# Performance work log

Measured on AMD Instinct MI355X. Metric: run time of the kernel, lower is better.

## Reference

```python
import jax, jax.numpy as jnp
import numpy as np

TAU_PRE = 2.0
TAU_POST = 2.0


def setup_inputs() -> dict:
    key = jax.random.key(0)
    k1, k2, k3 = jax.random.split(key, 3)
    T, B, PRE, POST = 64, 16, 4096, 4096
    in_spikes = jax.random.uniform(k1, (T, B, PRE), dtype=jnp.float32)
    out_spikes = jax.random.uniform(k2, (T, B, POST), dtype=jnp.float32)
    weight = jax.random.normal(k3, (POST, PRE), dtype=jnp.float32)
    return {"in_spikes": in_spikes, "out_spikes": out_spikes, "weight": weight}


def reference(in_spikes, out_spikes, weight):
    # in_spikes: [T, B, pre]; out_spikes: [T, B, post]; weight: [post, pre]
    T, B, PRE = in_spikes.shape
    POST = out_spikes.shape[-1]

    def step(carry, xs):
        trace_pre, trace_post, delta_w = carry
        i_sp, o_sp = xs
        trace_pre = jnp.clip(trace_pre - trace_pre / TAU_PRE + i_sp, 0.0, 1.0)  # [B, pre]
        trace_post = trace_post - trace_post / TAU_POST + o_sp  # [B, post]
        # sum_b o[b,post]*trace_pre[b,pre] - (sum_b o[b,post]*trace_post[b,post]) * w[post,pre]
        dw = (jnp.einsum('bo,bp->op', o_sp, trace_pre)
              - (o_sp * trace_post).sum(0)[:, None] * weight)
        return (trace_pre, trace_post, delta_w + dw), None

    init = (jnp.zeros((B, PRE), in_spikes.dtype),
            jnp.zeros((B, POST), out_spikes.dtype),
            jnp.zeros((POST, PRE), weight.dtype))
    (trace_pre, trace_post, delta_w), _ = jax.lax.scan(step, init, (in_spikes, out_spikes))
    return delta_w
```

## Files before the change

kernel.cpp:

```cpp
#include <hip/hip_runtime.h>


#define T_STEPS 64
#define B_SZ    16
#define PRE     4096
#define POST    4096
#define K_TOT   1024

typedef __attribute__((ext_vector_type(8))) unsigned short ushort8;
typedef __attribute__((ext_vector_type(8))) __bf16 bf16x8;
typedef __attribute__((ext_vector_type(4))) float floatx4;

__device__ __forceinline__ unsigned short f2bf(float f) {
    unsigned int u = __float_as_uint(f);
    u += 0x7fff + ((u >> 16) & 1);
    return (unsigned short)(u >> 16);
}

__device__ __forceinline__ void glds16(const void* g, void* l) {
    __builtin_amdgcn_global_load_lds((const __attribute__((address_space(1))) void*)g,
                                     (__attribute__((address_space(3))) void*)l,
                                     16, 0, 0);
}

__global__ __launch_bounds__(256) void trace_convert(
        const float* __restrict__ in_spikes,
        const float* __restrict__ out_spikes,
        unsigned short* __restrict__ AT,
        unsigned short* __restrict__ BT,
        float* __restrict__ coef) {
    __shared__ float ldsf[4096];
    __shared__ unsigned short ot[128 * 34];
    __shared__ float cbuf[8][33];
    const int tid  = threadIdx.x;
    const int wave = tid >> 6;
    const int lane = tid & 63;
    const bool isA = blockIdx.x >= 128;
    const int p0 = (blockIdx.x & 127) * 32;
    const float* src = isA ? out_spikes : in_spikes;
    unsigned short* dst = isA ? AT : BT;

    const int bA = tid >> 5;
    const int pA = tid & 31;

    float st0 = 0.f, st1 = 0.f, c0 = 0.f, c1 = 0.f;

    for (int tc = 0; tc < 8; ++tc) {
        const int T0 = tc * 8;
        #pragma unroll
        for (int i = 0; i < 4; ++i) {
            const int q  = (wave * 4 + i) * 64 + lane;
            const int p  = (q & 7) * 4;
            const int b  = (q >> 3) & 15;
            const int tl = q >> 7;
            const float* g = src + ((size_t)((T0 + tl) * 16 + b)) * 4096 + p0 + p;
            glds16(g, (char*)ldsf + (size_t)(wave * 4 + i) * 1024);
        }
        __syncthreads();

        #pragma unroll
        for (int tl = 0; tl < 8; ++tl) {
            const float x0 = ldsf[tl * 512 + bA * 32 + pA];
            const float x1 = ldsf[tl * 512 + (bA + 8) * 32 + pA];
            if (isA) {
                st0 = 0.5f * st0 + x0; c0 += x0 * st0;
                st1 = 0.5f * st1 + x1; c1 += x1 * st1;
                ot[(tl * 16 + bA)     * 34 + pA] = f2bf(x0);
                ot[(tl * 16 + bA + 8) * 34 + pA] = f2bf(x1);
            } else {
                st0 = fminf(fmaxf(0.5f * st0 + x0, 0.f), 1.f);
                st1 = fminf(fmaxf(0.5f * st1 + x1, 0.f), 1.f);
                ot[(tl * 16 + bA)     * 34 + pA] = f2bf(st0);
                ot[(tl * 16 + bA + 8) * 34 + pA] = f2bf(st1);
            }
        }
        __syncthreads();

        const int pf = tid >> 3;
        const int c8 = tid & 7;
        #pragma unroll
        for (int i = 0; i < 2; ++i) {
            const int ch = c8 + i * 8;
            ushort8 v;
            #pragma unroll
            for (int s = 0; s < 8; ++s) v[s] = ot[(ch * 8 + s) * 34 + pf];
            *(ushort8*)&dst[(size_t)(p0 + pf) * K_TOT + T0 * 16 + ch * 8] = v;
        }
    }

    if (isA) {
        cbuf[bA][pA] = c0 + c1;
        __syncthreads();
        if (tid < 32) {
            float s = 0.f;
            #pragma unroll
            for (int r = 0; r < 8; ++r) s += cbuf[r][tid];
            coef[p0 + tid] = s;
        }
    }
}

#define BK 64

__global__ __launch_bounds__(256) void stdp_gemm_mfma(
        const unsigned short* __restrict__ AT,
        const unsigned short* __restrict__ BT,
        const float* __restrict__ W,
        const float* __restrict__ coef,
        float* __restrict__ Cout) {
    __shared__ unsigned short As[128][BK];
    __shared__ unsigned short Bs[128][BK];
    const int tid  = threadIdx.x;
    const int lane = tid & 63;
    const int wave = tid >> 6;
    const int wm = (wave >> 1) * 64;
    const int wn = (wave & 1) * 64;
    const int m0 = blockIdx.y * 128;
    const int n0 = blockIdx.x * 128;

    floatx4 acc[4][4];
    #pragma unroll
    for (int i = 0; i < 4; ++i)
        #pragma unroll
        for (int j = 0; j < 4; ++j)
            acc[i][j] = (floatx4){0.f, 0.f, 0.f, 0.f};

    const int srow = tid >> 3;
    const int qg   = (tid & 7) ^ (srow & 7);
    const unsigned short* ga = &AT[(size_t)(m0 + srow) * K_TOT + qg * 8];
    const unsigned short* gb = &BT[(size_t)(n0 + srow) * K_TOT + qg * 8];
    char* laB = (char*)&As[0][0] + wave * 1024;
    char* lbB = (char*)&Bs[0][0] + wave * 1024;

    const int rm = lane & 15;
    const int q  = lane >> 4;
    const int sw = rm & 7;

    for (int k0 = 0; k0 < K_TOT; k0 += BK) {
        #pragma unroll
        for (int i = 0; i < 4; ++i) {
            glds16(ga + (size_t)i * 32 * K_TOT, laB + i * 4096);
            glds16(gb + (size_t)i * 32 * K_TOT, lbB + i * 4096);
        }
        ga += BK; gb += BK;
        __syncthreads();

        #pragma unroll
        for (int h = 0; h < 2; ++h) {
            const int ks = ((h * 4 + q) ^ sw) * 8;
            bf16x8 af[4], bv[4];
            #pragma unroll
            for (int i = 0; i < 4; ++i) {
                af[i] = *(const bf16x8*)&As[wm + i * 16 + rm][ks];
                bv[i] = *(const bf16x8*)&Bs[wn + i * 16 + rm][ks];
            }
            #pragma unroll
            for (int mi = 0; mi < 4; ++mi)
                #pragma unroll
                for (int ni = 0; ni < 4; ++ni)
                    acc[mi][ni] = __builtin_amdgcn_mfma_f32_16x16x32_bf16(
                        af[mi], bv[ni], acc[mi][ni], 0, 0, 0);
        }
        __syncthreads();
    }

    const int colp = n0 + wn + rm;
    const int rowb = m0 + wm + (lane >> 4) * 4;
    #pragma unroll
    for (int mi = 0; mi < 4; ++mi) {
        #pragma unroll
        for (int r = 0; r < 4; ++r) {
            const int o = rowb + mi * 16 + r;
            const float cf = coef[o];
            const float* wr = &W[(size_t)o * PRE];
            float* cr = &Cout[(size_t)o * PRE];
            #pragma unroll
            for (int ni = 0; ni < 4; ++ni) {
                const int p = colp + ni * 16;
                cr[p] = acc[mi][ni][r] - cf * wr[p];
            }
        }
    }
}

extern "C" void kernel_launch(void* const* d_in, const int* in_sizes, int n_in,
                              void* d_out, int out_size, void* d_ws, size_t ws_size,
                              hipStream_t stream) {
    const float* in_spikes  = (const float*)d_in[0];
    const float* out_spikes = (const float*)d_in[1];
    const float* weight     = (const float*)d_in[2];
    float* out = (float*)d_out;

    unsigned short* AT = (unsigned short*)d_ws;
    unsigned short* BT = AT + (size_t)POST * K_TOT;
    float* coef = (float*)(BT + (size_t)PRE * K_TOT);

    trace_convert<<<256, 256, 0, stream>>>(in_spikes, out_spikes, AT, BT, coef);

    dim3 grid(PRE / 128, POST / 128);
    stdp_gemm_mfma<<<grid, 256, 0, stream>>>(AT, BT, weight, coef, out);
}
```

Before: 184.3 us.

## Triple-buffer GEMM K-loop with 256x128 tiles and prefetched weight epilogue

Restructures the MFMA GEMM into 512-thread blocks covering 256x128 output tiles. A three-stage LDS ring is filled via global_load_lds, with explicit vmcnt waits and raw barriers in place of double syncthreads. Part of the weight rows used in the epilogue are prefetched into registers during early K tiles, and blocks are remapped with a swizzle for L2 locality. Waves get MFMA priority via setprio. The large LDS footprint limits occupancy to one block per CU, and the hand-tuned vmcnt counts are fragile.

```diff
diff --git a/kernel.cpp b/kernel.cpp
--- a/kernel.cpp
+++ b/kernel.cpp
@@ -101,22 +101,30 @@
 }
 
 #define BK 64
-
-__global__ __launch_bounds__(256) void stdp_gemm_mfma(
+#define NTILES (K_TOT / BK)
+
+__global__ __launch_bounds__(512, 2) void stdp_gemm_mfma(
         const unsigned short* __restrict__ AT,
         const unsigned short* __restrict__ BT,
         const float* __restrict__ W,
         const float* __restrict__ coef,
         float* __restrict__ Cout) {
-    __shared__ unsigned short As[128][BK];
-    __shared__ unsigned short Bs[128][BK];
+    __shared__ __align__(16) char lds[3][49152];
+
     const int tid  = threadIdx.x;
     const int lane = tid & 63;
     const int wave = tid >> 6;
+
+    const int bid = blockIdx.x;
+    const int f   = (bid & 7) * 64 + (bid >> 3);
+    const int m0  = (f >> 5) * 256;
+    const int n0  = (f & 31) * 128;
+
     const int wm = (wave >> 1) * 64;
     const int wn = (wave & 1) * 64;
-    const int m0 = blockIdx.y * 128;
-    const int n0 = blockIdx.x * 128;
+    const int rm = lane & 15;
+    const int q  = lane >> 4;
+    const int sw = rm & 7;
 
     floatx4 acc[4][4];
     #pragma unroll
@@ -124,60 +132,83 @@
         #pragma unroll
         for (int j = 0; j < 4; ++j)
             acc[i][j] = (floatx4){0.f, 0.f, 0.f, 0.f};
+    float wr[8][4];
 
     const int srow = tid >> 3;
     const int qg   = (tid & 7) ^ (srow & 7);
     const unsigned short* ga = &AT[(size_t)(m0 + srow) * K_TOT + qg * 8];
     const unsigned short* gb = &BT[(size_t)(n0 + srow) * K_TOT + qg * 8];
-    char* laB = (char*)&As[0][0] + wave * 1024;
-    char* lbB = (char*)&Bs[0][0] + wave * 1024;
-
-    const int rm = lane & 15;
-    const int q  = lane >> 4;
-    const int sw = rm & 7;
-
-    for (int k0 = 0; k0 < K_TOT; k0 += BK) {
-        #pragma unroll
-        for (int i = 0; i < 4; ++i) {
-            glds16(ga + (size_t)i * 32 * K_TOT, laB + i * 4096);
-            glds16(gb + (size_t)i * 32 * K_TOT, lbB + i * 4096);
-        }
-        ga += BK; gb += BK;
-        __syncthreads();
-
+    const int colp = n0 + wn + rm;
+
+    auto STAGE = [&](int t) {
+        char* base = (char*)&lds[t % 3][0] + wave * 1024;
+        const unsigned short* gaT = ga + t * BK;
+        const unsigned short* gbT = gb + t * BK;
+        #pragma unroll
+        for (int i = 0; i < 4; ++i)
+            glds16(gaT + (size_t)i * 64 * K_TOT, base + i * 8192);
+        #pragma unroll
+        for (int i = 0; i < 2; ++i)
+            glds16(gbT + (size_t)i * 64 * K_TOT, base + 32768 + i * 8192);
+    };
+
+    STAGE(0);
+    asm volatile("" ::: "memory");
+    STAGE(1);
+    asm volatile("s_waitcnt vmcnt(6)" ::: "memory");
+    __builtin_amdgcn_s_barrier();
+    __builtin_amdgcn_sched_barrier(0);
+
+    #pragma unroll
+    for (int t = 0; t < NTILES; ++t) {
+        if (t + 2 < NTILES) STAGE(t + 2);
+        if (t < 8) {
+            const int o = m0 + wm + q * 4 + (t >> 2) * 16 + (t & 3);
+            const float* wrow = &W[(size_t)o * PRE + colp];
+            #pragma unroll
+            for (int ni = 0; ni < 4; ++ni) wr[t][ni] = wrow[ni * 16];
+        }
+        const char* Ab = (const char*)&lds[t % 3][0];
+        const char* Bb = Ab + 32768;
         #pragma unroll
         for (int h = 0; h < 2; ++h) {
-            const int ks = ((h * 4 + q) ^ sw) * 8;
             bf16x8 af[4], bv[4];
             #pragma unroll
             for (int i = 0; i < 4; ++i) {
-                af[i] = *(const bf16x8*)&As[wm + i * 16 + rm][ks];
-                bv[i] = *(const bf16x8*)&Bs[wn + i * 16 + rm][ks];
+                const int ks = ((h * 4 + q) ^ sw) * 16;
+                af[i] = *(const bf16x8*)(Ab + (wm + i * 16 + rm) * 128 + ks);
+                bv[i] = *(const bf16x8*)(Bb + (wn + i * 16 + rm) * 128 + ks);
             }
+            __builtin_amdgcn_s_setprio(1);
             #pragma unroll
             for (int mi = 0; mi < 4; ++mi)
                 #pragma unroll
                 for (int ni = 0; ni < 4; ++ni)
                     acc[mi][ni] = __builtin_amdgcn_mfma_f32_16x16x32_bf16(
                         af[mi], bv[ni], acc[mi][ni], 0, 0, 0);
-        }
-        __syncthreads();
-    }
-
-    const int colp = n0 + wn + rm;
-    const int rowb = m0 + wm + (lane >> 4) * 4;
+            __builtin_amdgcn_s_setprio(0);
+        }
+        if (t < NTILES - 1) {
+            if (t < 8)       asm volatile("s_waitcnt vmcnt(10)" ::: "memory");
+            else if (t < 14) asm volatile("s_waitcnt vmcnt(6)"  ::: "memory");
+            else             asm volatile("s_waitcnt vmcnt(0)"  ::: "memory");
+            __builtin_amdgcn_s_barrier();
+            __builtin_amdgcn_sched_barrier(0);
+        }
+    }
+
     #pragma unroll
     for (int mi = 0; mi < 4; ++mi) {
         #pragma unroll
         for (int r = 0; r < 4; ++r) {
-            const int o = rowb + mi * 16 + r;
+            const int o = m0 + wm + q * 4 + mi * 16 + r;
             const float cf = coef[o];
-            const float* wr = &W[(size_t)o * PRE];
-            float* cr = &Cout[(size_t)o * PRE];
+            const float* wrow = &W[(size_t)o * PRE + colp];
+            float* crow = &Cout[(size_t)o * PRE + colp];
             #pragma unroll
             for (int ni = 0; ni < 4; ++ni) {
-                const int p = colp + ni * 16;
-                cr[p] = acc[mi][ni][r] - cf * wr[p];
+                const float wv = (mi < 2) ? wr[mi * 4 + r][ni] : wrow[ni * 16];
+                crow[ni * 16] = acc[mi][ni][r] - cf * wv;
             }
         }
     }
@@ -197,6 +228,5 @@
 
     trace_convert<<<256, 256, 0, stream>>>(in_spikes, out_spikes, AT, BT, coef);
 
-    dim3 grid(PRE / 128, POST / 128);
-    stdp_gemm_mfma<<<grid, 256, 0, stream>>>(AT, BT, weight, coef, out);
-}
+    stdp_gemm_mfma<<<512, 512, 0, stream>>>(AT, BT, weight, coef, out);
+}
```

New measurement: 184.5 us. About the same (+0.1%).

## Rewrite GEMM with 256x256 tiles and double-buffered phased LDS pipeline

Applied to the files above, without the earlier changes.

Replaces the 128x128 single-buffered GEMM with 256x256 tiles per 512-thread block, using a 128KB double-buffered LDS scheme. Loads are issued in interleaved phases with explicit vmcnt waits, barriers and setprio, so global-to-LDS transfers overlap MFMA work. A block-index remap groups tiles for cache locality, and a new XOR swizzle avoids bank conflicts. The larger tile doubles register pressure for accumulators and limits occupancy to one block per CU.

```diff
diff --git a/kernel.cpp b/kernel.cpp
--- a/kernel.cpp
+++ b/kernel.cpp
@@ -100,87 +100,122 @@
     }
 }
 
-#define BK 64
-
-__global__ __launch_bounds__(256) void stdp_gemm_mfma(
+#define NTILES 16
+
+#define LOFF(buf, isB, kh) ((buf) * 65536 + (isB) * 32768 + (kh) * 16384)
+
+__global__ __launch_bounds__(512, 2) void stdp_gemm_mfma(
         const unsigned short* __restrict__ AT,
         const unsigned short* __restrict__ BT,
         const float* __restrict__ W,
         const float* __restrict__ coef,
         float* __restrict__ Cout) {
-    __shared__ unsigned short As[128][BK];
-    __shared__ unsigned short Bs[128][BK];
+    __shared__ __align__(16) char ldsraw[131072];
+
     const int tid  = threadIdx.x;
     const int lane = tid & 63;
     const int wave = tid >> 6;
-    const int wm = (wave >> 1) * 64;
-    const int wn = (wave & 1) * 64;
-    const int m0 = blockIdx.y * 128;
-    const int n0 = blockIdx.x * 128;
-
-    floatx4 acc[4][4];
+
+    const int bid = blockIdx.x;
+    const int f   = (bid & 7) * 32 + (bid >> 3);
+    const int m0  = (f >> 4) * 256;
+    const int n0  = (f & 15) * 256;
+
+    const int wm  = (wave >> 2) * 128;
+    const int wn  = (wave & 3) * 64;
+    const int rml = lane & 15;
+    const int q   = lane >> 4;
+    const int swz16 = ((q ^ ((rml >> 1) & 3)) << 4);
+
+    floatx4 acc[8][4];
     #pragma unroll
-    for (int i = 0; i < 4; ++i)
+    for (int i = 0; i < 8; ++i)
         #pragma unroll
         for (int j = 0; j < 4; ++j)
             acc[i][j] = (floatx4){0.f, 0.f, 0.f, 0.f};
-
-    const int srow = tid >> 3;
-    const int qg   = (tid & 7) ^ (srow & 7);
-    const unsigned short* ga = &AT[(size_t)(m0 + srow) * K_TOT + qg * 8];
-    const unsigned short* gb = &BT[(size_t)(n0 + srow) * K_TOT + qg * 8];
-    char* laB = (char*)&As[0][0] + wave * 1024;
-    char* lbB = (char*)&Bs[0][0] + wave * 1024;
-
-    const int rm = lane & 15;
-    const int q  = lane >> 4;
-    const int sw = rm & 7;
-
-    for (int k0 = 0; k0 < K_TOT; k0 += BK) {
-        #pragma unroll
-        for (int i = 0; i < 4; ++i) {
-            glds16(ga + (size_t)i * 32 * K_TOT, laB + i * 4096);
-            glds16(gb + (size_t)i * 32 * K_TOT, lbB + i * 4096);
-        }
-        ga += BK; gb += BK;
-        __syncthreads();
-
-        #pragma unroll
-        for (int h = 0; h < 2; ++h) {
-            const int ks = ((h * 4 + q) ^ sw) * 8;
-            bf16x8 af[4], bv[4];
+    bf16x8 bv[4];
+
+    const int cid0 = wave * 64 + lane;
+    const int row0 = cid0 >> 2;
+    const int g0   = (cid0 & 3) ^ ((row0 >> 1) & 3);
+    const unsigned short* gA0 = AT + (size_t)(m0 + row0) * K_TOT + g0 * 8;
+    const unsigned short* gB0 = BT + (size_t)(n0 + row0) * K_TOT + g0 * 8;
+
+    #define STG(isB, t, kh)                                                        \
+        do {                                                                       \
+            const unsigned short* s0_ = ((isB) ? gB0 : gA0) + (t) * 64 + (kh) * 32;\
+            char* d_ = ldsraw + LOFF((t) & 1, (isB), (kh)) + wave * 1024;          \
+            glds16(s0_, d_);                                                       \
+            glds16(s0_ + (size_t)128 * K_TOT, d_ + 8192);                          \
+        } while (0)
+
+    #define PHASE(bufc, khc, mqc, SISB, ST, SKH, SCOND, WM)                        \
+        do {                                                                       \
+            const char* Ab_ = ldsraw + LOFF(bufc, 0, khc);                         \
+            const char* Bb_ = ldsraw + LOFF(bufc, 1, khc);                         \
+            if ((mqc) == 0) {                                                      \
+                _Pragma("unroll")                                                  \
+                for (int ni = 0; ni < 4; ++ni)                                     \
+                    bv[ni] = *(const bf16x8*)(Bb_ + (wn + ni * 16 + rml) * 64 + swz16); \
+            }                                                                      \
+            bf16x8 af_[4];                                                         \
+            _Pragma("unroll")                                                      \
+            for (int k4 = 0; k4 < 4; ++k4)                                         \
+                af_[k4] = *(const bf16x8*)(Ab_ + (wm + (mqc) * 64 + k4 * 16 + rml) * 64 + swz16); \
+            if (SCOND) STG(SISB, ST, SKH);                                         \
+            if ((WM) == 1)      asm volatile("s_waitcnt vmcnt(4)" ::: "memory");   \
+            else if ((WM) == 2) asm volatile("s_waitcnt vmcnt(0)" ::: "memory");   \
+            __builtin_amdgcn_s_barrier();                                          \
+            __builtin_amdgcn_sched_barrier(0);                                     \
+            __builtin_amdgcn_s_setprio(1);                                         \
+            _Pragma("unroll")                                                      \
+            for (int k4 = 0; k4 < 4; ++k4)                                         \
+                _Pragma("unroll")                                                  \
+                for (int ni = 0; ni < 4; ++ni)                                     \
+                    acc[(mqc) * 4 + k4][ni] = __builtin_amdgcn_mfma_f32_16x16x32_bf16( \
+                        af_[k4], bv[ni], acc[(mqc) * 4 + k4][ni], 0, 0, 0);        \
+            __builtin_amdgcn_s_setprio(0);                                         \
+            __builtin_amdgcn_s_barrier();                                          \
+            __builtin_amdgcn_sched_barrier(0);                                     \
+        } while (0)
+
+    STG(0, 0, 0); STG(1, 0, 0); STG(0, 0, 1); STG(1, 0, 1);
+    STG(0, 1, 0); STG(1, 1, 0); STG(0, 1, 1); STG(1, 1, 1);
+    asm volatile("s_waitcnt vmcnt(8)" ::: "memory");
+    __builtin_amdgcn_s_barrier();
+    __builtin_amdgcn_sched_barrier(0);
+
+    for (int i = 0; i < 8; ++i) {
+        const int t2 = 2 * i + 2, t3 = 2 * i + 3, tA = 2 * i + 1;
+        const int wm4 = (i < 7) ? 1 : 2;
+        const int wm8 = (i < 7) ? 1 : 0;
+        PHASE(0, 0, 0, 0, tA, 1, i > 0,      0);
+        PHASE(0, 0, 1, 1, tA, 1, i > 0,      0);
+        PHASE(0, 1, 0, 0, t2, 0, t2 < NTILES, 0);
+        PHASE(0, 1, 1, 1, t2, 0, t2 < NTILES, wm4);
+        PHASE(1, 0, 0, 0, t2, 1, t2 < NTILES, 0);
+        PHASE(1, 0, 1, 1, t2, 1, t2 < NTILES, 0);
+        PHASE(1, 1, 0, 0, t3, 0, t3 < NTILES, 0);
+        PHASE(1, 1, 1, 1, t3, 0, t3 < NTILES, wm8);
+    }
+
+    const int colp = n0 + wn + rml;
+    const int q4   = lane >> 4;
+    #pragma unroll
+    for (int mi = 0; mi < 8; ++mi) {
+        #pragma unroll
+        for (int r = 0; r < 4; ++r) {
+            const int o = m0 + wm + mi * 16 + q4 * 4 + r;
+            const float cf = coef[o];
+            const float* wrow = &W[(size_t)o * PRE + colp];
+            float* crow = &Cout[(size_t)o * PRE + colp];
             #pragma unroll
-            for (int i = 0; i < 4; ++i) {
-                af[i] = *(const bf16x8*)&As[wm + i * 16 + rm][ks];
-                bv[i] = *(const bf16x8*)&Bs[wn + i * 16 + rm][ks];
-            }
-            #pragma unroll
-            for (int mi = 0; mi < 4; ++mi)
-                #pragma unroll
-                for (int ni = 0; ni < 4; ++ni)
-                    acc[mi][ni] = __builtin_amdgcn_mfma_f32_16x16x32_bf16(
-                        af[mi], bv[ni], acc[mi][ni], 0, 0, 0);
-        }
-        __syncthreads();
-    }
-
-    const int colp = n0 + wn + rm;
-    const int rowb = m0 + wm + (lane >> 4) * 4;
-    #pragma unroll
-    for (int mi = 0; mi < 4; ++mi) {
-        #pragma unroll
-        for (int r = 0; r < 4; ++r) {
-            const int o = rowb + mi * 16 + r;
-            const float cf = coef[o];
-            const float* wr = &W[(size_t)o * PRE];
-            float* cr = &Cout[(size_t)o * PRE];
-            #pragma unroll
-            for (int ni = 0; ni < 4; ++ni) {
-                const int p = colp + ni * 16;
-                cr[p] = acc[mi][ni][r] - cf * wr[p];
-            }
-        }
-    }
+            for (int ni = 0; ni < 4; ++ni)
+                crow[ni * 16] = acc[mi][ni][r] - cf * wrow[ni * 16];
+        }
+    }
+    #undef PHASE
+    #undef STG
 }
 
 extern "C" void kernel_launch(void* const* d_in, const int* in_sizes, int n_in,
@@ -197,6 +232,5 @@
 
     trace_convert<<<256, 256, 0, stream>>>(in_spikes, out_spikes, AT, BT, coef);
 
-    dim3 grid(PRE / 128, POST / 128);
-    stdp_gemm_mfma<<<grid, 256, 0, stream>>>(AT, BT, weight, coef, out);
-}
+    stdp_gemm_mfma<<<256, 512, 0, stream>>>(AT, BT, weight, coef, out);
+}
```

Result: no change. 180.8 us (-1.9%).
